# Kernel optimization log

Measured on AMD Instinct MI355X. Metric: run time of the kernel, lower is better.

## Reference

```python
import jax, jax.numpy as jnp
import numpy as np

N_HEADS = 16


def setup_inputs() -> dict:
    key = jax.random.key(0)
    ks = jax.random.split(key, 7)
    B, S, D = 2, 2048, 1024
    x = jax.random.normal(ks[0], (B, S, D), dtype=jnp.float32)
    attn_mask = jax.random.normal(ks[1], (S, S), dtype=jnp.float32) * 0.1
    attn_bias = jax.random.normal(ks[2], (B, S, S), dtype=jnp.float32) * 0.1
    Wqkv = jax.random.normal(ks[3], (D, 3 * D), dtype=jnp.float32) * (D ** -0.5)
    bqkv = jnp.zeros((3 * D,), dtype=jnp.float32)
    Wout = jax.random.normal(ks[4], (D, D), dtype=jnp.float32) * (D ** -0.5)
    bout = jnp.zeros((D,), dtype=jnp.float32)
    return {"x": x, "attn_mask": attn_mask, "attn_bias": attn_bias,
            "Wqkv": Wqkv, "bqkv": bqkv, "Wout": Wout, "bout": bout}


def reference(x, attn_mask, attn_bias, Wqkv, bqkv, Wout, bout):
    B, S, D = x.shape
    H = N_HEADS
    hd = D // H
    # qkv projection: [B,S,3D] -> [3,B,H,S,hd]
    qkv = (x @ Wqkv + bqkv).reshape(B, S, 3, H, hd).transpose(2, 0, 3, 1, 4)
    q, k, v = qkv[0], qkv[1], qkv[2]
    scores = jnp.einsum('bhqd,bhkd->bhqk', q, k) / (hd ** 0.5)
    scores = scores + attn_mask[None, None, :, :] + attn_bias[:, None, :, :]
    attn = jax.nn.softmax(scores, axis=-1)  # dropout p=0.0 (eval)
    out = jnp.einsum('bhqk,bhkd->bhqd', attn, v)
    out = out.transpose(0, 2, 1, 3).reshape(B, S, D)
    return out @ Wout + bout
```

## Files before the change

kernel.cpp:

```cpp
#include <hip/hip_runtime.h>
#include <hip/hip_bf16.h>


#define S_LEN 2048
#define DMODEL 1024
#define NH 16
#define HD 64

typedef __bf16 bf16x8 __attribute__((ext_vector_type(8)));
typedef __bf16 bf16x4 __attribute__((ext_vector_type(4)));
typedef __bf16 bf16x2v __attribute__((ext_vector_type(2)));
typedef float f32x4 __attribute__((ext_vector_type(4)));
typedef short s16x4 __attribute__((ext_vector_type(4)));

#define GLD_LDS16(g, l)                                              \
  __builtin_amdgcn_global_load_lds(                                  \
      (const __attribute__((address_space(1))) unsigned int*)(g),    \
      (__attribute__((address_space(3))) unsigned int*)(l), 16, 0, 0)

#if __has_builtin(__builtin_amdgcn_mfma_f32_16x16x16bf16_1k)
#define HAVE_MFMA_16x16x16_BF16 1
#else
#define HAVE_MFMA_16x16x16_BF16 0
#endif

#if __has_builtin(__builtin_amdgcn_exp2f)
#define EXP2F(x) __builtin_amdgcn_exp2f(x)
#else
static __device__ __forceinline__ float EXP2F(float x) {
  float r;
  asm volatile("v_exp_f32 %0, %1" : "=v"(r) : "v"(x));
  return r;
}
#endif

#define LOG2E 1.44269504f

__global__ __launch_bounds__(256) void preprocess(
    const float* __restrict__ x, const float* __restrict__ mask,
    const float* __restrict__ bias, const float* __restrict__ Wqkv,
    const float* __restrict__ Wout, __bf16* __restrict__ Xb,
    __bf16* __restrict__ Wt, __bf16* __restrict__ Wt2,
    __bf16* __restrict__ MB) {
  __shared__ __align__(16) char smem[64 * 65 * 4];
  const int bid = blockIdx.x;
  const int tid = threadIdx.x;

  if (bid < 4096) {
    int i = bid * 256 + tid;
    float4 v = ((const float4*)x)[i];
    bf16x4 o = {(__bf16)v.x, (__bf16)v.y, (__bf16)v.z, (__bf16)v.w};
    *(bf16x4*)&Xb[(size_t)i * 4] = o;
  } else if (bid < 5120) {
    const float* W;
    __bf16* Wo;
    int ncols, n0, k0;
    if (bid < 4864) {
      int id = bid - 4096;
      W = Wqkv; Wo = Wt; ncols = 3072;
      n0 = (id % 48) * 64; k0 = (id / 48) * 64;
    } else {
      int id = bid - 4864;
      W = Wout; Wo = Wt2; ncols = 1024;
      n0 = (id & 15) * 64; k0 = (id >> 4) * 64;
    }
    float(*tile)[65] = (float(*)[65])smem;
    {
      int c = tid & 63, r4 = tid >> 6;
#pragma unroll
      for (int p = 0; p < 16; ++p) {
        int r = r4 + p * 4;
        tile[r][c] = W[(size_t)(k0 + r) * ncols + n0 + c];
      }
    }
    __syncthreads();
    {
      int cc = (tid & 31) * 2, r8 = tid >> 5;
#pragma unroll
      for (int p = 0; p < 8; ++p) {
        int rr = r8 + p * 8;
        bf16x2v o = {(__bf16)tile[cc][rr], (__bf16)tile[cc + 1][rr]};
        *(bf16x2v*)&Wo[(size_t)(n0 + rr) * 1024 + k0 + cc] = o;
      }
    }
  } else {
    int id = bid - 5120;
    const int kt = id & 31, qt = id >> 5;
    __bf16(*sm)[68] = (__bf16(*)[68])smem;
    const int r0 = tid >> 4;
    const int cc = (tid & 15) * 4;
    const float* mrow = mask + (size_t)(qt * 64) * S_LEN + kt * 64;
    float4 mld[4];
#pragma unroll
    for (int p = 0; p < 4; ++p)
      mld[p] = *(const float4*)(mrow + (size_t)(r0 + p * 16) * S_LEN + cc);
    const int w = tid >> 6, lane = tid & 63;
    const int quad = lane >> 4, cl = lane & 15;
    for (int b = 0; b < 2; ++b) {
      const float* brow =
          bias + ((size_t)b * S_LEN + qt * 64) * S_LEN + kt * 64;
#pragma unroll
      for (int p = 0; p < 4; ++p) {
        int r = r0 + p * 16;
        float4 a = *(const float4*)(brow + (size_t)r * S_LEN + cc);
        sm[r][cc + 0] = (__bf16)((mld[p].x + a.x) * LOG2E);
        sm[r][cc + 1] = (__bf16)((mld[p].y + a.y) * LOG2E);
        sm[r][cc + 2] = (__bf16)((mld[p].z + a.z) * LOG2E);
        sm[r][cc + 3] = (__bf16)((mld[p].w + a.w) * LOG2E);
      }
      __syncthreads();
      __bf16 vals[16];
#pragma unroll
      for (int ct = 0; ct < 4; ++ct) {
        bf16x4 v = *(const bf16x4*)&sm[w * 16 + cl][ct * 16 + quad * 4];
        *(bf16x4*)&vals[ct * 4] = v;
      }
      __bf16* op = MB + (((size_t)(b * 32 + qt) * 32 + kt) * 4096) +
                   (w * 64 + lane) * 16;
      *(bf16x8*)op = *(bf16x8*)&vals[0];
      *(bf16x8*)(op + 8) = *(bf16x8*)&vals[8];
      __syncthreads();
    }
  }
}

__global__ __launch_bounds__(256) void gemm_qkv_mfma(
    const __bf16* __restrict__ Xb, const __bf16* __restrict__ Wt,
    const float* __restrict__ bqkv, __bf16* __restrict__ Qb,
    __bf16* __restrict__ Kb, __bf16* __restrict__ Vtb) {
  __shared__ __align__(16) __bf16 As[128 * 32];
  __shared__ __align__(16) __bf16 Bs[128 * 32];
  const int tid = threadIdx.x;
  const int w = tid >> 6, lane = tid & 63;
  const int c = lane & 15, quad = lane >> 4;
  const int wm = w >> 1, wn = w & 1;
  const int rowBase = blockIdx.y * 128;
  const int colBase = blockIdx.x * 128;

  f32x4 acc[4][4] = {};

  const __bf16* gA0 =
      Xb + (size_t)(rowBase + w * 32 + (lane >> 2)) * 1024 + (lane & 3) * 8;
  const __bf16* gB0 =
      Wt + (size_t)(colBase + w * 32 + (lane >> 2)) * 1024 + (lane & 3) * 8;
  __bf16* lA0 = &As[(w * 32) * 32];
  __bf16* lB0 = &Bs[(w * 32) * 32];

  for (int k0 = 0; k0 < 1024; k0 += 32) {
    __syncthreads();
#pragma unroll
    for (int p = 0; p < 2; ++p) {
      GLD_LDS16(gA0 + (size_t)p * 16 * 1024 + k0, lA0 + p * 16 * 32);
      GLD_LDS16(gB0 + (size_t)p * 16 * 1024 + k0, lB0 + p * 16 * 32);
    }
    __syncthreads();

    bf16x8 af[4], bfr[4];
#pragma unroll
    for (int mt = 0; mt < 4; ++mt)
      af[mt] = *(const bf16x8*)&As[(wm * 64 + mt * 16 + c) * 32 + quad * 8];
#pragma unroll
    for (int nt = 0; nt < 4; ++nt)
      bfr[nt] = *(const bf16x8*)&Bs[(wn * 64 + nt * 16 + c) * 32 + quad * 8];
#pragma unroll
    for (int mt = 0; mt < 4; ++mt)
#pragma unroll
      for (int nt = 0; nt < 4; ++nt)
        acc[mt][nt] = __builtin_amdgcn_mfma_f32_16x16x32_bf16(
            af[mt], bfr[nt], acc[mt][nt], 0, 0, 0);
  }

#pragma unroll
  for (int mt = 0; mt < 4; ++mt) {
    int row0 = rowBase + wm * 64 + mt * 16 + quad * 4;
#pragma unroll
    for (int nt = 0; nt < 4; ++nt) {
      int col = colBase + wn * 64 + nt * 16 + c;
      float bias = bqkv[col];
      int three = col >> 10;
      int h = (col & 1023) >> 6;
      int d = col & 63;
#pragma unroll
      for (int r = 0; r < 4; ++r) {
        int rr = row0 + r;
        int bb = rr >> 11, s = rr & 2047;
        float val = acc[mt][nt][r] + bias;
        size_t ho = (size_t)(bb * NH + h);
        if (three == 0)
          Qb[(ho * S_LEN + s) * HD + d] = (__bf16)val;
        else if (three == 1)
          Kb[(ho * S_LEN + s) * HD + d] = (__bf16)val;
        else
          Vtb[(ho * HD + d) * S_LEN + s] = (__bf16)val;
      }
    }
  }
}

__global__ __launch_bounds__(256) void attn_mfma(
    const __bf16* __restrict__ Qb, const __bf16* __restrict__ Kb,
    const __bf16* __restrict__ Vtb, const __bf16* __restrict__ MB,
    __bf16* __restrict__ AOb) {
  const int qt = blockIdx.x, h = blockIdx.y, b = blockIdx.z;
  const int tid = threadIdx.x;
  const int w = tid >> 6;
  const int lane = tid & 63;
  const int c = lane & 15;
  const int quad = lane >> 4;

  __shared__ __align__(16) __bf16 Ks[2][2][64 * 64];
  __shared__ __align__(16) __bf16 Vs[2][2][64 * 64];
#if !HAVE_MFMA_16x16x16_BF16
  __shared__ __align__(16) __bf16 P2[4][16 * 72];
#endif

  const size_t headoff = (size_t)(b * NH + h) * S_LEN * HD;
  const __bf16* Qg = Qb + headoff + (size_t)(qt * 128) * HD;
  const __bf16* Kg = Kb + headoff;
  const __bf16* Vg = Vtb + headoff;
  const __bf16* MBq0 =
      MB + ((size_t)(b * 32 + qt * 2 + 0) * 32) * 4096 + (w * 64 + lane) * 16;
  const __bf16* MBq1 =
      MB + ((size_t)(b * 32 + qt * 2 + 1) * 32) * 4096 + (w * 64 + lane) * 16;

  const int f0 = tid >> 3, f1 = f0 + 32;
  const int j = tid & 7;
  const int sj0 = j ^ (f0 & 7);
  const int sj1 = j ^ (f1 & 7);
  const int lds0 = tid * 8;
  const int lds1 = (256 + tid) * 8;

  bf16x8 qa[2][2];
#pragma unroll
  for (int g = 0; g < 2; ++g) {
    qa[g][0] = *(const bf16x8*)(Qg + (g * 64 + w * 16 + c) * HD + quad * 8);
    qa[g][1] =
        *(const bf16x8*)(Qg + (g * 64 + w * 16 + c) * HD + quad * 8 + 32);
  }

  const int rs0 = (quad ^ (c & 7)) * 8;
  const int rs1 = ((quad + 4) ^ (c & 7)) * 8;

  f32x4 Oa[2][4] = {};
  f32x4 psum[2] = {};

  const float c1 = 0.125f * LOG2E;

  auto subtile = [&](const __bf16* KsS, const __bf16* VsS,
                     bf16x8(&rmb)[2][2]) {
    bf16x8 kf0[4], kf1[4];
#pragma unroll
    for (int ct = 0; ct < 4; ++ct) {
      kf0[ct] = *(const bf16x8*)&KsS[(ct * 16 + c) * 64 + rs0];
      kf1[ct] = *(const bf16x8*)&KsS[(ct * 16 + c) * 64 + rs1];
    }
    f32x4 sv[2][4];
    __builtin_amdgcn_s_setprio(1);
#pragma unroll
    for (int g = 0; g < 2; ++g)
#pragma unroll
      for (int ct = 0; ct < 4; ++ct) {
        f32x4 a = {};
        a = __builtin_amdgcn_mfma_f32_16x16x32_bf16(kf0[ct], qa[g][0], a, 0,
                                                    0, 0);
        a = __builtin_amdgcn_mfma_f32_16x16x32_bf16(kf1[ct], qa[g][1], a, 0,
                                                    0, 0);
        sv[g][ct] = a;
      }
    __builtin_amdgcn_s_setprio(0);

#if HAVE_MFMA_16x16x16_BF16
    s16x4 vf[4][4];
#pragma unroll
    for (int ft = 0; ft < 4; ++ft) {
      const int fr = ft * 16 + c;
#pragma unroll
      for (int ct = 0; ct < 4; ++ct) {
        const int chunk = ((ct * 2 + (quad >> 1)) ^ (fr & 7)) * 8 +
                          (quad & 1) * 4;
        vf[ft][ct] = *(const s16x4*)&VsS[fr * 64 + chunk];
      }
    }
#endif

    s16x4 pb[2][4];
#pragma unroll
    for (int g = 0; g < 2; ++g)
#pragma unroll
      for (int ct = 0; ct < 4; ++ct) {
        f32x4 pv;
#pragma unroll
        for (int r = 0; r < 4; ++r) {
          float mb = (ct < 2) ? (float)rmb[g][0][ct * 4 + r]
                              : (float)rmb[g][1][(ct - 2) * 4 + r];
          pv[r] = EXP2F(sv[g][ct][r] * c1 + mb);
        }
        psum[g] += pv;
        __bf16 t4[4];
#pragma unroll
        for (int r = 0; r < 4; ++r) t4[r] = (__bf16)pv[r];
        pb[g][ct] = *(s16x4*)t4;
      }

#if HAVE_MFMA_16x16x16_BF16
    __builtin_amdgcn_s_setprio(1);
#pragma unroll
    for (int g = 0; g < 2; ++g)
#pragma unroll
      for (int ft = 0; ft < 4; ++ft)
#pragma unroll
        for (int ct = 0; ct < 4; ++ct)
          Oa[g][ft] = __builtin_amdgcn_mfma_f32_16x16x16bf16_1k(
              vf[ft][ct], pb[g][ct], Oa[g][ft], 0, 0, 0);
    __builtin_amdgcn_s_setprio(0);
#else
#pragma unroll
    for (int g = 0; g < 2; ++g) {
#pragma unroll
      for (int ct = 0; ct < 4; ++ct)
        *(bf16x4*)&P2[w][c * 72 + ct * 16 + quad * 4] = *(bf16x4*)&pb[g][ct];
      bf16x8 pf0 = *(const bf16x8*)&P2[w][c * 72 + quad * 8];
      bf16x8 pf1 = *(const bf16x8*)&P2[w][c * 72 + 32 + quad * 8];
#pragma unroll
      for (int ft = 0; ft < 4; ++ft) {
        const int fr = ft * 16 + c;
        bf16x8 vf0 = *(const bf16x8*)&VsS[fr * 64 + rs0];
        bf16x8 vf1 = *(const bf16x8*)&VsS[fr * 64 + rs1];
        Oa[g][ft] = __builtin_amdgcn_mfma_f32_16x16x32_bf16(vf0, pf0,
                                                            Oa[g][ft], 0, 0, 0);
        Oa[g][ft] = __builtin_amdgcn_mfma_f32_16x16x32_bf16(vf1, pf1,
                                                            Oa[g][ft], 0, 0, 0);
      }
    }
#endif
  };

  GLD_LDS16(Kg + (size_t)f0 * HD + sj0 * 8, &Ks[0][0][lds0]);
  GLD_LDS16(Kg + (size_t)f1 * HD + sj1 * 8, &Ks[0][0][lds1]);
  GLD_LDS16(Kg + (size_t)(64 + f0) * HD + sj0 * 8, &Ks[0][1][lds0]);
  GLD_LDS16(Kg + (size_t)(64 + f1) * HD + sj1 * 8, &Ks[0][1][lds1]);
  GLD_LDS16(Vg + (size_t)f0 * S_LEN + sj0 * 8, &Vs[0][0][lds0]);
  GLD_LDS16(Vg + (size_t)f1 * S_LEN + sj1 * 8, &Vs[0][0][lds1]);
  GLD_LDS16(Vg + (size_t)f0 * S_LEN + 64 + sj0 * 8, &Vs[0][1][lds0]);
  GLD_LDS16(Vg + (size_t)f1 * S_LEN + 64 + sj1 * 8, &Vs[0][1][lds1]);

  const __bf16* kgp0 = Kg + (size_t)(128 + f0) * HD + sj0 * 8;
  const __bf16* kgp1 = Kg + (size_t)(128 + f1) * HD + sj1 * 8;
  const __bf16* vgp0 = Vg + (size_t)f0 * S_LEN + 128 + sj0 * 8;
  const __bf16* vgp1 = Vg + (size_t)f1 * S_LEN + 128 + sj1 * 8;

  bf16x8 rMBA[2][2], rMBB[2][2];
  rMBA[0][0] = *(const bf16x8*)MBq0;
  rMBA[0][1] = *(const bf16x8*)(MBq0 + 8);
  rMBA[1][0] = *(const bf16x8*)MBq1;
  rMBA[1][1] = *(const bf16x8*)(MBq1 + 8);
  rMBB[0][0] = *(const bf16x8*)(MBq0 + 4096);
  rMBB[0][1] = *(const bf16x8*)(MBq0 + 4096 + 8);
  rMBB[1][0] = *(const bf16x8*)(MBq1 + 4096);
  rMBB[1][1] = *(const bf16x8*)(MBq1 + 4096 + 8);

  __syncthreads();

#pragma unroll 2
  for (int t = 0; t < 16; ++t) {
    const int cur = t & 1, nxt = cur ^ 1;
    if (t < 15) {
      GLD_LDS16(kgp0, &Ks[nxt][0][lds0]);
      GLD_LDS16(kgp1, &Ks[nxt][0][lds1]);
      GLD_LDS16(kgp0 + 64 * HD, &Ks[nxt][1][lds0]);
      GLD_LDS16(kgp1 + 64 * HD, &Ks[nxt][1][lds1]);
      GLD_LDS16(vgp0, &Vs[nxt][0][lds0]);
      GLD_LDS16(vgp1, &Vs[nxt][0][lds1]);
      GLD_LDS16(vgp0 + 64, &Vs[nxt][1][lds0]);
      GLD_LDS16(vgp1 + 64, &Vs[nxt][1][lds1]);
    }
    kgp0 += 128 * HD;
    kgp1 += 128 * HD;
    vgp0 += 128;
    vgp1 += 128;

    subtile(&Ks[cur][0][0], &Vs[cur][0][0], rMBA);

    bf16x8 nMBA[2][2], nMBB[2][2];
    {
      const __bf16* m0 = MBq0 + (size_t)(2 * t + 2) * 4096;
      const __bf16* m1 = MBq1 + (size_t)(2 * t + 2) * 4096;
      nMBA[0][0] = *(const bf16x8*)m0;
      nMBA[0][1] = *(const bf16x8*)(m0 + 8);
      nMBA[1][0] = *(const bf16x8*)m1;
      nMBA[1][1] = *(const bf16x8*)(m1 + 8);
      nMBB[0][0] = *(const bf16x8*)(m0 + 4096);
      nMBB[0][1] = *(const bf16x8*)(m0 + 4096 + 8);
      nMBB[1][0] = *(const bf16x8*)(m1 + 4096);
      nMBB[1][1] = *(const bf16x8*)(m1 + 4096 + 8);
    }

    subtile(&Ks[cur][1][0], &Vs[cur][1][0], rMBB);

#pragma unroll
    for (int g = 0; g < 2; ++g) {
      rMBA[g][0] = nMBA[g][0];
      rMBA[g][1] = nMBA[g][1];
      rMBB[g][0] = nMBB[g][0];
      rMBB[g][1] = nMBB[g][1];
    }

    __syncthreads();
  }

#pragma unroll
  for (int g = 0; g < 2; ++g) {
    float lsum = psum[g][0] + psum[g][1] + psum[g][2] + psum[g][3];
    lsum += __shfl_xor(lsum, 16);
    lsum += __shfl_xor(lsum, 32);
    const float invl = 1.0f / lsum;
    __bf16* orow = AOb +
                   (size_t)(b * S_LEN + qt * 128 + g * 64 + w * 16 + c) *
                       DMODEL +
                   h * HD;
#pragma unroll
    for (int ft = 0; ft < 4; ++ft) {
      __bf16 t4[4];
#pragma unroll
      for (int r = 0; r < 4; ++r) t4[r] = (__bf16)(Oa[g][ft][r] * invl);
      *(bf16x4*)(orow + ft * 16 + quad * 4) = *(bf16x4*)t4;
    }
  }
}

__global__ __launch_bounds__(256) void gemm_out_mfma(
    const __bf16* __restrict__ AOb, const __bf16* __restrict__ Wt2,
    const float* __restrict__ bout, float* __restrict__ Out) {
  __shared__ __align__(16) __bf16 As[128 * 32];
  __shared__ __align__(16) __bf16 Bs[64 * 32];
  const int tid = threadIdx.x;
  const int w = tid >> 6, lane = tid & 63;
  const int c = lane & 15, quad = lane >> 4;
  const int rowBase = blockIdx.y * 128;
  const int colBase = blockIdx.x * 64;

  f32x4 acc[2][4] = {};

  const __bf16* gA0 =
      AOb + (size_t)(rowBase + w * 32 + (lane >> 2)) * 1024 + (lane & 3) * 8;
  const __bf16* gB0 =
      Wt2 + (size_t)(colBase + w * 16 + (lane >> 2)) * 1024 + (lane & 3) * 8;
  __bf16* lA0 = &As[(w * 32) * 32];
  __bf16* lB0 = &Bs[(w * 16) * 32];

  for (int k0 = 0; k0 < 1024; k0 += 32) {
    __syncthreads();
#pragma unroll
    for (int p = 0; p < 2; ++p)
      GLD_LDS16(gA0 + (size_t)p * 16 * 1024 + k0, lA0 + p * 16 * 32);
    GLD_LDS16(gB0 + k0, lB0);
    __syncthreads();

    bf16x8 af[2], bfr[4];
#pragma unroll
    for (int mt = 0; mt < 2; ++mt)
      af[mt] = *(const bf16x8*)&As[(w * 32 + mt * 16 + c) * 32 + quad * 8];
#pragma unroll
    for (int nt = 0; nt < 4; ++nt)
      bfr[nt] = *(const bf16x8*)&Bs[(nt * 16 + c) * 32 + quad * 8];
#pragma unroll
    for (int mt = 0; mt < 2; ++mt)
#pragma unroll
      for (int nt = 0; nt < 4; ++nt)
        acc[mt][nt] = __builtin_amdgcn_mfma_f32_16x16x32_bf16(
            af[mt], bfr[nt], acc[mt][nt], 0, 0, 0);
  }

#pragma unroll
  for (int mt = 0; mt < 2; ++mt) {
    int row0 = rowBase + w * 32 + mt * 16 + quad * 4;
#pragma unroll
    for (int nt = 0; nt < 4; ++nt) {
      int col = colBase + nt * 16 + c;
      float bias = bout[col];
#pragma unroll
      for (int r = 0; r < 4; ++r)
        Out[(size_t)(row0 + r) * 1024 + col] = acc[mt][nt][r] + bias;
    }
  }
}

extern "C" void kernel_launch(void* const* d_in, const int* in_sizes, int n_in,
                              void* d_out, int out_size, void* d_ws,
                              size_t ws_size, hipStream_t stream) {
  const float* x = (const float*)d_in[0];
  const float* attn_mask = (const float*)d_in[1];
  const float* attn_bias = (const float*)d_in[2];
  const float* Wqkv = (const float*)d_in[3];
  const float* bqkv = (const float*)d_in[4];
  const float* Wout = (const float*)d_in[5];
  const float* bout = (const float*)d_in[6];
  float* out = (float*)d_out;

  __bf16* base = (__bf16*)d_ws;
  __bf16* Xb = base;
  __bf16* AOb = base;
  __bf16* Wt = base + 4194304;
  __bf16* Qb = base + 8388608;
  __bf16* Kb = base + 12582912;
  __bf16* Vtb = base + 16777216;
  __bf16* MB = base + 20971520;
  __bf16* Wt2 = base + 29360128;

  preprocess<<<6144, 256, 0, stream>>>(x, attn_mask, attn_bias, Wqkv, Wout,
                                       Xb, Wt, Wt2, MB);
  gemm_qkv_mfma<<<dim3(24, 32), 256, 0, stream>>>(Xb, Wt, bqkv, Qb, Kb, Vtb);
  attn_mfma<<<dim3(16, NH, 2), 256, 0, stream>>>(Qb, Kb, Vtb, MB, AOb);
  gemm_out_mfma<<<dim3(16, 32), 256, 0, stream>>>(AOb, Wt2, bout, out);
}
```

Before: 270.8 us.

## Stage QKV epilogue through LDS for coalesced stores; interleave QK and softmax per group

The QKV GEMM epilogue now writes each wave's 64x64 tile into padded LDS (reusing the A/B staging buffers) and then emits 16-byte coalesced stores to Q/K or transposed V, replacing scattered 2-byte stores. For V the tile is transposed in LDS so rows along S are contiguous. In the attention kernel the per-group QK MFMA and exp/softmax steps are interleaved, and the mask-bias prefetch for the next tile is issued inside the subtile right after use, cutting live registers for sv and the separate nMB arrays. The costs are an extra LDS round trip plus a barrier in the GEMM, and possibly less latency hiding for the mask loads.

```diff
diff --git a/kernel.cpp b/kernel.cpp
--- a/kernel.cpp
+++ b/kernel.cpp
@@ -128,8 +128,9 @@
     const __bf16* __restrict__ Xb, const __bf16* __restrict__ Wt,
     const float* __restrict__ bqkv, __bf16* __restrict__ Qb,
     __bf16* __restrict__ Kb, __bf16* __restrict__ Vtb) {
-  __shared__ __align__(16) __bf16 As[128 * 32];
-  __shared__ __align__(16) __bf16 Bs[128 * 32];
+  __shared__ __align__(16) __bf16 shm[4 * 64 * 80];
+  __bf16* As = shm;
+  __bf16* Bs = shm + 4096;
   const int tid = threadIdx.x;
   const int w = tid >> 6, lane = tid & 63;
   const int c = lane & 15, quad = lane >> 4;
@@ -170,29 +171,58 @@
             af[mt], bfr[nt], acc[mt][nt], 0, 0, 0);
   }
 
-#pragma unroll
-  for (int mt = 0; mt < 4; ++mt) {
-    int row0 = rowBase + wm * 64 + mt * 16 + quad * 4;
+  __syncthreads();
+  __bf16* Tt = shm + w * (64 * 80);
+  const int cols0 = colBase + wn * 64;
+  const int rows0 = rowBase + wm * 64;
+  const int three = colBase >> 10;
+  const int hq = (cols0 & 1023) >> 6;
+  const int bb = rows0 >> 11;
+  const int sBase = rows0 & 2047;
+
+  if (three < 2) {
 #pragma unroll
     for (int nt = 0; nt < 4; ++nt) {
-      int col = colBase + wn * 64 + nt * 16 + c;
-      float bias = bqkv[col];
-      int three = col >> 10;
-      int h = (col & 1023) >> 6;
-      int d = col & 63;
-#pragma unroll
-      for (int r = 0; r < 4; ++r) {
-        int rr = row0 + r;
-        int bb = rr >> 11, s = rr & 2047;
-        float val = acc[mt][nt][r] + bias;
-        size_t ho = (size_t)(bb * NH + h);
-        if (three == 0)
-          Qb[(ho * S_LEN + s) * HD + d] = (__bf16)val;
-        else if (three == 1)
-          Kb[(ho * S_LEN + s) * HD + d] = (__bf16)val;
-        else
-          Vtb[(ho * HD + d) * S_LEN + s] = (__bf16)val;
-      }
+      float bias = bqkv[cols0 + nt * 16 + c];
+#pragma unroll
+      for (int mt = 0; mt < 4; ++mt)
+#pragma unroll
+        for (int r = 0; r < 4; ++r)
+          Tt[(mt * 16 + quad * 4 + r) * 80 + nt * 16 + c] =
+              (__bf16)(acc[mt][nt][r] + bias);
+    }
+    __bf16* qk = three ? Kb : Qb;
+    const size_t rbase =
+        ((size_t)(bb * NH + hq) * S_LEN + sBase) * HD;
+    const int d8 = (lane & 7) * 8;
+    const int sl0 = lane >> 3;
+#pragma unroll
+    for (int i = 0; i < 8; ++i) {
+      int sl = sl0 + i * 8;
+      bf16x8 v = *(const bf16x8*)&Tt[sl * 80 + d8];
+      *(bf16x8*)&qk[rbase + (size_t)sl * HD + d8] = v;
+    }
+  } else {
+#pragma unroll
+    for (int nt = 0; nt < 4; ++nt) {
+      float bias = bqkv[cols0 + nt * 16 + c];
+#pragma unroll
+      for (int mt = 0; mt < 4; ++mt) {
+        __bf16 t4[4];
+#pragma unroll
+        for (int r = 0; r < 4; ++r) t4[r] = (__bf16)(acc[mt][nt][r] + bias);
+        *(bf16x4*)&Tt[(nt * 16 + c) * 80 + mt * 16 + quad * 4] =
+            *(bf16x4*)t4;
+      }
+    }
+    const size_t vbase = ((size_t)(bb * NH + hq) * HD) * S_LEN;
+    const int s0 = (lane & 7) * 8;
+    const int dl0 = lane >> 3;
+#pragma unroll
+    for (int dt = 0; dt < 8; ++dt) {
+      int dl = dt * 8 + dl0;
+      bf16x8 v = *(const bf16x8*)&Tt[dl * 80 + s0];
+      *(bf16x8*)&Vtb[vbase + (size_t)dl * S_LEN + sBase + s0] = v;
     }
   }
 }
@@ -247,17 +277,19 @@
   const float c1 = 0.125f * LOG2E;
 
   auto subtile = [&](const __bf16* KsS, const __bf16* VsS,
-                     bf16x8(&rmb)[2][2]) {
+                     bf16x8(&rmb)[2][2], const __bf16* mbn0,
+                     const __bf16* mbn1) {
     bf16x8 kf0[4], kf1[4];
 #pragma unroll
     for (int ct = 0; ct < 4; ++ct) {
       kf0[ct] = *(const bf16x8*)&KsS[(ct * 16 + c) * 64 + rs0];
       kf1[ct] = *(const bf16x8*)&KsS[(ct * 16 + c) * 64 + rs1];
     }
-    f32x4 sv[2][4];
-    __builtin_amdgcn_s_setprio(1);
-#pragma unroll
-    for (int g = 0; g < 2; ++g)
+    s16x4 pb[2][4];
+#pragma unroll
+    for (int g = 0; g < 2; ++g) {
+      f32x4 sv[4];
+      __builtin_amdgcn_s_setprio(1);
 #pragma unroll
       for (int ct = 0; ct < 4; ++ct) {
         f32x4 a = {};
@@ -265,9 +297,28 @@
                                                     0, 0);
         a = __builtin_amdgcn_mfma_f32_16x16x32_bf16(kf1[ct], qa[g][1], a, 0,
                                                     0, 0);
-        sv[g][ct] = a;
-      }
-    __builtin_amdgcn_s_setprio(0);
+        sv[ct] = a;
+      }
+      __builtin_amdgcn_s_setprio(0);
+#pragma unroll
+      for (int ct = 0; ct < 4; ++ct) {
+        f32x4 pv;
+#pragma unroll
+        for (int r = 0; r < 4; ++r) {
+          float mb = (ct < 2) ? (float)rmb[g][0][ct * 4 + r]
+                              : (float)rmb[g][1][(ct - 2) * 4 + r];
+          pv[r] = EXP2F(sv[ct][r] * c1 + mb);
+        }
+        psum[g] += pv;
+        __bf16 t4[4];
+#pragma unroll
+        for (int r = 0; r < 4; ++r) t4[r] = (__bf16)pv[r];
+        pb[g][ct] = *(s16x4*)t4;
+      }
+      const __bf16* mp = g ? mbn1 : mbn0;
+      rmb[g][0] = *(const bf16x8*)mp;
+      rmb[g][1] = *(const bf16x8*)(mp + 8);
+    }
 
 #if HAVE_MFMA_16x16x16_BF16
     s16x4 vf[4][4];
@@ -281,28 +332,6 @@
         vf[ft][ct] = *(const s16x4*)&VsS[fr * 64 + chunk];
       }
     }
-#endif
-
-    s16x4 pb[2][4];
-#pragma unroll
-    for (int g = 0; g < 2; ++g)
-#pragma unroll
-      for (int ct = 0; ct < 4; ++ct) {
-        f32x4 pv;
-#pragma unroll
-        for (int r = 0; r < 4; ++r) {
-          float mb = (ct < 2) ? (float)rmb[g][0][ct * 4 + r]
-                              : (float)rmb[g][1][(ct - 2) * 4 + r];
-          pv[r] = EXP2F(sv[g][ct][r] * c1 + mb);
-        }
-        psum[g] += pv;
-        __bf16 t4[4];
-#pragma unroll
-        for (int r = 0; r < 4; ++r) t4[r] = (__bf16)pv[r];
-        pb[g][ct] = *(s16x4*)t4;
-      }
-
-#if HAVE_MFMA_16x16x16_BF16
     __builtin_amdgcn_s_setprio(1);
 #pragma unroll
     for (int g = 0; g < 2; ++g)
@@ -324,11 +353,11 @@
 #pragma unroll
       for (int ft = 0; ft < 4; ++ft) {
         const int fr = ft * 16 + c;
-        bf16x8 vf0 = *(const bf16x8*)&VsS[fr * 64 + rs0];
-        bf16x8 vf1 = *(const bf16x8*)&VsS[fr * 64 + rs1];
-        Oa[g][ft] = __builtin_amdgcn_mfma_f32_16x16x32_bf16(vf0, pf0,
+        bf16x8 vv0 = *(const bf16x8*)&VsS[fr * 64 + rs0];
+        bf16x8 vv1 = *(const bf16x8*)&VsS[fr * 64 + rs1];
+        Oa[g][ft] = __builtin_amdgcn_mfma_f32_16x16x32_bf16(vv0, pf0,
                                                             Oa[g][ft], 0, 0, 0);
-        Oa[g][ft] = __builtin_amdgcn_mfma_f32_16x16x32_bf16(vf1, pf1,
+        Oa[g][ft] = __builtin_amdgcn_mfma_f32_16x16x32_bf16(vv1, pf1,
                                                             Oa[g][ft], 0, 0, 0);
       }
     }
@@ -379,31 +408,12 @@
     vgp0 += 128;
     vgp1 += 128;
 
-    subtile(&Ks[cur][0][0], &Vs[cur][0][0], rMBA);
-
-    bf16x8 nMBA[2][2], nMBB[2][2];
-    {
-      const __bf16* m0 = MBq0 + (size_t)(2 * t + 2) * 4096;
-      const __bf16* m1 = MBq1 + (size_t)(2 * t + 2) * 4096;
-      nMBA[0][0] = *(const bf16x8*)m0;
-      nMBA[0][1] = *(const bf16x8*)(m0 + 8);
-      nMBA[1][0] = *(const bf16x8*)m1;
-      nMBA[1][1] = *(const bf16x8*)(m1 + 8);
-      nMBB[0][0] = *(const bf16x8*)(m0 + 4096);
-      nMBB[0][1] = *(const bf16x8*)(m0 + 4096 + 8);
-      nMBB[1][0] = *(const bf16x8*)(m1 + 4096);
-      nMBB[1][1] = *(const bf16x8*)(m1 + 4096 + 8);
-    }
-
-    subtile(&Ks[cur][1][0], &Vs[cur][1][0], rMBB);
-
-#pragma unroll
-    for (int g = 0; g < 2; ++g) {
-      rMBA[g][0] = nMBA[g][0];
-      rMBA[g][1] = nMBA[g][1];
-      rMBB[g][0] = nMBB[g][0];
-      rMBB[g][1] = nMBB[g][1];
-    }
+    subtile(&Ks[cur][0][0], &Vs[cur][0][0], rMBA,
+            MBq0 + (size_t)(2 * t + 2) * 4096,
+            MBq1 + (size_t)(2 * t + 2) * 4096);
+    subtile(&Ks[cur][1][0], &Vs[cur][1][0], rMBB,
+            MBq0 + (size_t)(2 * t + 3) * 4096,
+            MBq1 + (size_t)(2 * t + 3) * 4096);
 
     __syncthreads();
   }
```

After: 258.5 us. 1.05x faster.

## Double-buffer LDS in projection GEMMs and transpose V epilogue via shared memory

Applied to the files above, without the earlier changes.

Both the QKV and output-projection GEMMs now prefetch the next K-slice into a second LDS buffer while computing on the current one, which drops to one barrier per iteration. The aim is to hide global-to-LDS load latency behind the MFMA work. The QKV epilogue also changes for the V columns: each wave stages its tile in LDS and writes the transposed V with 16-byte contiguous stores instead of scattered 2-byte strided writes. The cost is extra LDS use, which may lower occupancy.

```diff
diff --git a/kernel.cpp b/kernel.cpp
--- a/kernel.cpp
+++ b/kernel.cpp
@@ -128,8 +128,9 @@
     const __bf16* __restrict__ Xb, const __bf16* __restrict__ Wt,
     const float* __restrict__ bqkv, __bf16* __restrict__ Qb,
     __bf16* __restrict__ Kb, __bf16* __restrict__ Vtb) {
-  __shared__ __align__(16) __bf16 As[128 * 32];
-  __shared__ __align__(16) __bf16 Bs[128 * 32];
+  __shared__ __align__(16) __bf16 shm[4 * 64 * 72];
+  __bf16* As = shm;
+  __bf16* Bs = shm + 8192;
   const int tid = threadIdx.x;
   const int w = tid >> 6, lane = tid & 63;
   const int c = lane & 15, quad = lane >> 4;
@@ -143,56 +144,99 @@
       Xb + (size_t)(rowBase + w * 32 + (lane >> 2)) * 1024 + (lane & 3) * 8;
   const __bf16* gB0 =
       Wt + (size_t)(colBase + w * 32 + (lane >> 2)) * 1024 + (lane & 3) * 8;
-  __bf16* lA0 = &As[(w * 32) * 32];
-  __bf16* lB0 = &Bs[(w * 32) * 32];
-
+  const int lOff = (w * 32) * 32;
+
+#pragma unroll
+  for (int p = 0; p < 2; ++p) {
+    GLD_LDS16(gA0 + (size_t)p * 16 * 1024, As + lOff + p * 16 * 32);
+    GLD_LDS16(gB0 + (size_t)p * 16 * 1024, Bs + lOff + p * 16 * 32);
+  }
+  __syncthreads();
+
+#pragma unroll 2
   for (int k0 = 0; k0 < 1024; k0 += 32) {
-    __syncthreads();
-#pragma unroll
-    for (int p = 0; p < 2; ++p) {
-      GLD_LDS16(gA0 + (size_t)p * 16 * 1024 + k0, lA0 + p * 16 * 32);
-      GLD_LDS16(gB0 + (size_t)p * 16 * 1024 + k0, lB0 + p * 16 * 32);
-    }
-    __syncthreads();
+    const int cur = (k0 >> 5) & 1, nxt = cur ^ 1;
+    if (k0 < 992) {
+#pragma unroll
+      for (int p = 0; p < 2; ++p) {
+        GLD_LDS16(gA0 + (size_t)p * 16 * 1024 + k0 + 32,
+                  As + nxt * 4096 + lOff + p * 16 * 32);
+        GLD_LDS16(gB0 + (size_t)p * 16 * 1024 + k0 + 32,
+                  Bs + nxt * 4096 + lOff + p * 16 * 32);
+      }
+    }
 
     bf16x8 af[4], bfr[4];
 #pragma unroll
     for (int mt = 0; mt < 4; ++mt)
-      af[mt] = *(const bf16x8*)&As[(wm * 64 + mt * 16 + c) * 32 + quad * 8];
+      af[mt] = *(const bf16x8*)&As[cur * 4096 +
+                                   (wm * 64 + mt * 16 + c) * 32 + quad * 8];
 #pragma unroll
     for (int nt = 0; nt < 4; ++nt)
-      bfr[nt] = *(const bf16x8*)&Bs[(wn * 64 + nt * 16 + c) * 32 + quad * 8];
+      bfr[nt] = *(const bf16x8*)&Bs[cur * 4096 +
+                                    (wn * 64 + nt * 16 + c) * 32 + quad * 8];
 #pragma unroll
     for (int mt = 0; mt < 4; ++mt)
 #pragma unroll
       for (int nt = 0; nt < 4; ++nt)
         acc[mt][nt] = __builtin_amdgcn_mfma_f32_16x16x32_bf16(
             af[mt], bfr[nt], acc[mt][nt], 0, 0, 0);
-  }
-
-#pragma unroll
-  for (int mt = 0; mt < 4; ++mt) {
-    int row0 = rowBase + wm * 64 + mt * 16 + quad * 4;
+
+    __syncthreads();
+  }
+
+  if (colBase < 2048) {
+#pragma unroll
+    for (int mt = 0; mt < 4; ++mt) {
+      int row0 = rowBase + wm * 64 + mt * 16 + quad * 4;
+#pragma unroll
+      for (int nt = 0; nt < 4; ++nt) {
+        int col = colBase + wn * 64 + nt * 16 + c;
+        float bias = bqkv[col];
+        int three = col >> 10;
+        int h = (col & 1023) >> 6;
+        int d = col & 63;
+#pragma unroll
+        for (int r = 0; r < 4; ++r) {
+          int rr = row0 + r;
+          int bb = rr >> 11, s = rr & 2047;
+          float val = acc[mt][nt][r] + bias;
+          size_t ho = (size_t)(bb * NH + h);
+          if (three == 0)
+            Qb[(ho * S_LEN + s) * HD + d] = (__bf16)val;
+          else
+            Kb[(ho * S_LEN + s) * HD + d] = (__bf16)val;
+        }
+      }
+    }
+  } else {
+    __bf16* Tt = shm + w * (64 * 72);
+    const int cols0 = colBase + wn * 64;
+    const int rows0 = rowBase + wm * 64;
+    const int hq = (cols0 & 1023) >> 6;
+    const int bb = rows0 >> 11;
+    const int sBase = rows0 & 2047;
 #pragma unroll
     for (int nt = 0; nt < 4; ++nt) {
-      int col = colBase + wn * 64 + nt * 16 + c;
-      float bias = bqkv[col];
-      int three = col >> 10;
-      int h = (col & 1023) >> 6;
-      int d = col & 63;
-#pragma unroll
-      for (int r = 0; r < 4; ++r) {
-        int rr = row0 + r;
-        int bb = rr >> 11, s = rr & 2047;
-        float val = acc[mt][nt][r] + bias;
-        size_t ho = (size_t)(bb * NH + h);
-        if (three == 0)
-          Qb[(ho * S_LEN + s) * HD + d] = (__bf16)val;
-        else if (three == 1)
-          Kb[(ho * S_LEN + s) * HD + d] = (__bf16)val;
-        else
-          Vtb[(ho * HD + d) * S_LEN + s] = (__bf16)val;
-      }
+      float bias = bqkv[cols0 + nt * 16 + c];
+#pragma unroll
+      for (int mt = 0; mt < 4; ++mt) {
+        __bf16 t4[4];
+#pragma unroll
+        for (int r = 0; r < 4; ++r) t4[r] = (__bf16)(acc[mt][nt][r] + bias);
+        *(bf16x4*)&Tt[(nt * 16 + c) * 72 + mt * 16 + quad * 4] =
+            *(bf16x4*)t4;
+      }
+    }
+    __syncthreads();
+    const size_t vbase = ((size_t)(bb * NH + hq) * HD) * S_LEN;
+    const int s0 = (lane & 7) * 8;
+    const int dl0 = lane >> 3;
+#pragma unroll
+    for (int dt = 0; dt < 8; ++dt) {
+      int dl = dt * 8 + dl0;
+      bf16x8 v = *(const bf16x8*)&Tt[dl * 72 + s0];
+      *(bf16x8*)&Vtb[vbase + (size_t)dl * S_LEN + sBase + s0] = v;
     }
   }
 }
@@ -324,11 +368,11 @@
 #pragma unroll
       for (int ft = 0; ft < 4; ++ft) {
         const int fr = ft * 16 + c;
-        bf16x8 vf0 = *(const bf16x8*)&VsS[fr * 64 + rs0];
-        bf16x8 vf1 = *(const bf16x8*)&VsS[fr * 64 + rs1];
-        Oa[g][ft] = __builtin_amdgcn_mfma_f32_16x16x32_bf16(vf0, pf0,
+        bf16x8 vv0 = *(const bf16x8*)&VsS[fr * 64 + rs0];
+        bf16x8 vv1 = *(const bf16x8*)&VsS[fr * 64 + rs1];
+        Oa[g][ft] = __builtin_amdgcn_mfma_f32_16x16x32_bf16(vv0, pf0,
                                                             Oa[g][ft], 0, 0, 0);
-        Oa[g][ft] = __builtin_amdgcn_mfma_f32_16x16x32_bf16(vf1, pf1,
+        Oa[g][ft] = __builtin_amdgcn_mfma_f32_16x16x32_bf16(vv1, pf1,
                                                             Oa[g][ft], 0, 0, 0);
       }
     }
@@ -431,8 +475,8 @@
 __global__ __launch_bounds__(256) void gemm_out_mfma(
     const __bf16* __restrict__ AOb, const __bf16* __restrict__ Wt2,
     const float* __restrict__ bout, float* __restrict__ Out) {
-  __shared__ __align__(16) __bf16 As[128 * 32];
-  __shared__ __align__(16) __bf16 Bs[64 * 32];
+  __shared__ __align__(16) __bf16 As[2][128 * 32];
+  __shared__ __align__(16) __bf16 Bs[2][64 * 32];
   const int tid = threadIdx.x;
   const int w = tid >> 6, lane = tid & 63;
   const int c = lane & 15, quad = lane >> 4;
@@ -445,30 +489,42 @@
       AOb + (size_t)(rowBase + w * 32 + (lane >> 2)) * 1024 + (lane & 3) * 8;
   const __bf16* gB0 =
       Wt2 + (size_t)(colBase + w * 16 + (lane >> 2)) * 1024 + (lane & 3) * 8;
-  __bf16* lA0 = &As[(w * 32) * 32];
-  __bf16* lB0 = &Bs[(w * 16) * 32];
-
+  const int lA = (w * 32) * 32;
+  const int lB = (w * 16) * 32;
+
+#pragma unroll
+  for (int p = 0; p < 2; ++p)
+    GLD_LDS16(gA0 + (size_t)p * 16 * 1024, &As[0][lA + p * 16 * 32]);
+  GLD_LDS16(gB0, &Bs[0][lB]);
+  __syncthreads();
+
+#pragma unroll 2
   for (int k0 = 0; k0 < 1024; k0 += 32) {
-    __syncthreads();
-#pragma unroll
-    for (int p = 0; p < 2; ++p)
-      GLD_LDS16(gA0 + (size_t)p * 16 * 1024 + k0, lA0 + p * 16 * 32);
-    GLD_LDS16(gB0 + k0, lB0);
-    __syncthreads();
+    const int cur = (k0 >> 5) & 1, nxt = cur ^ 1;
+    if (k0 < 992) {
+#pragma unroll
+      for (int p = 0; p < 2; ++p)
+        GLD_LDS16(gA0 + (size_t)p * 16 * 1024 + k0 + 32,
+                  &As[nxt][lA + p * 16 * 32]);
+      GLD_LDS16(gB0 + k0 + 32, &Bs[nxt][lB]);
+    }
 
     bf16x8 af[2], bfr[4];
 #pragma unroll
     for (int mt = 0; mt < 2; ++mt)
-      af[mt] = *(const bf16x8*)&As[(w * 32 + mt * 16 + c) * 32 + quad * 8];
+      af[mt] =
+          *(const bf16x8*)&As[cur][(w * 32 + mt * 16 + c) * 32 + quad * 8];
 #pragma unroll
     for (int nt = 0; nt < 4; ++nt)
-      bfr[nt] = *(const bf16x8*)&Bs[(nt * 16 + c) * 32 + quad * 8];
+      bfr[nt] = *(const bf16x8*)&Bs[cur][(nt * 16 + c) * 32 + quad * 8];
 #pragma unroll
     for (int mt = 0; mt < 2; ++mt)
 #pragma unroll
       for (int nt = 0; nt < 4; ++nt)
         acc[mt][nt] = __builtin_amdgcn_mfma_f32_16x16x32_bf16(
             af[mt], bfr[nt], acc[mt][nt], 0, 0, 0);
+
+    __syncthreads();
   }
 
 #pragma unroll
```

Result: faster. 252.5 us (-6.8%).
